# Kernel tuning notes

Hardware: AMD Instinct MI355X
Metric: run time of the kernel (lower is better)

## Reference

```python
import jax, jax.numpy as jnp
import numpy as np

NUM_HEADS = 8
KEY_DIM = 512  # d_gain = 1/sqrt(key_dim) in the original (NOT per-head dim)
MASK_FILL = -1000000.0


def setup_inputs() -> dict:
    key = jax.random.key(0)
    ks = jax.random.split(key, 6)
    N, Tq, Tk, D, U = 8, 1024, 1024, 512, 512
    query = jax.random.normal(ks[0], (N, Tq, D), dtype=jnp.float32)
    key_t = jax.random.normal(ks[1], (N, Tk, D), dtype=jnp.float32)
    key_mask = jax.random.randint(ks[2], (N, Tk), 0, 2).astype(bool)
    Wq = jax.random.normal(ks[3], (D, U), dtype=jnp.float32) / np.sqrt(D)
    Wk = jax.random.normal(ks[4], (D, U), dtype=jnp.float32) / np.sqrt(D)
    Wv = jax.random.normal(ks[5], (D, U), dtype=jnp.float32) / np.sqrt(D)
    return {"query": query, "key": key_t, "key_mask": key_mask,
            "Wq": Wq, "Wk": Wk, "Wv": Wv}


def reference(query, key, key_mask, Wq, Wk, Wv):
    N, Tq, _ = query.shape
    Tk = key.shape[1]
    U = Wq.shape[1]
    h = NUM_HEADS
    d = U // h
    scale = 1.0 / (KEY_DIM ** 0.5)

    # projections then split heads: [N,T,U] -> [h,N,T,d]
    q = (query @ Wq).reshape(N, Tq, h, d).transpose(2, 0, 1, 3)
    k = (key @ Wk).reshape(N, Tk, h, d).transpose(2, 0, 1, 3)
    v = (key @ Wv).reshape(N, Tk, h, d).transpose(2, 0, 1, 3)

    scores = scale * jnp.einsum('hnqd,hnkd->hnqk', q, k)
    scores = jnp.where(key_mask[None, :, None, :], scores, MASK_FILL)
    attn = jax.nn.softmax(scores, axis=3)
    out = jnp.einsum('hnqk,hnkd->hnqd', attn, v)
    # merge heads: [h,N,Tq,d] -> [N,Tq,h*d]
    return out.transpose(1, 2, 0, 3).reshape(N, Tq, U)
```

## Files before the change

### kernel.cpp

```cpp
#include <hip/hip_runtime.h>
#include <hip/hip_bf16.h>

typedef unsigned short u16;
typedef __attribute__((ext_vector_type(8))) short short8;
typedef __attribute__((ext_vector_type(4))) short short4v;
typedef __attribute__((ext_vector_type(4))) float f32x4;

#define NB 8
#define TT 1024
#define DD 512
#define UU 512
#define HH 8
#define DH 64
#define SCALE 0.044194173824159216f
#define LOG2E 1.4426950408889634f
#define MASK_FILL_2 -1442695.0f

__device__ __forceinline__ float ld_flex(const void* p, long i, bool f32) {
  if (f32) return ((const float*)p)[i];
  unsigned int u = (unsigned int)(((const u16*)p)[i]) << 16;
  return __uint_as_float(u);
}

__device__ __forceinline__ u16 f32_to_bf16(float f) {
  unsigned int u = __float_as_uint(f);
  unsigned int r = (u + 0x7FFFu + ((u >> 16) & 1u)) >> 16;
  return (u16)r;
}

__device__ __forceinline__ float ex2(float x) {
#if __has_builtin(__builtin_amdgcn_exp2f)
  return __builtin_amdgcn_exp2f(x);
#else
  return __expf(x * 0.6931471805599453f);
#endif
}

__device__ __forceinline__ unsigned int pk_bf16(float a, float b) {
  union { __hip_bfloat162 h2; unsigned int u; } c;
  c.h2 = __float22bfloat162_rn(make_float2(a, b));
  return c.u;
}

__device__ __forceinline__ void gld16(const void* g, void* l) {
  __builtin_amdgcn_global_load_lds(
      (const __attribute__((address_space(1))) unsigned int*)g,
      (__attribute__((address_space(3))) unsigned int*)l, 16, 0, 0);
}

#define CONV_BLOCKS 8192
#define WT_BLOCKS 768
#define MASK_BLOCKS 32

__global__ __launch_bounds__(256) void prep_kernel(
    const void* __restrict__ query, const void* __restrict__ key,
    const void* __restrict__ W0, const void* __restrict__ W1,
    const void* __restrict__ W2, const void* __restrict__ mask,
    u16* __restrict__ Xq, u16* __restrict__ Xk, u16* __restrict__ Wt,
    float* __restrict__ maskadd, int* __restrict__ flags) {
  __shared__ float tile[32][33];
  __shared__ int s_f32, s_mi32;
  const int b = blockIdx.x, tid = threadIdx.x;

  if (tid == 0) { s_f32 = 0; s_mi32 = 1; }
  __syncthreads();
  {
    const u16* qh = (const u16*)query;
    int weird = 0;
#pragma unroll
    for (int p = 0; p < 4; ++p) {
      unsigned int u = (unsigned int)qh[tid * 4 + p] << 16;
      float v = __uint_as_float(u);
      if (!(v == v) || fabsf(v) > 1e6f) weird = 1;
    }
    if (weird) atomicOr(&s_f32, 1);
    const unsigned int* mi = (const unsigned int*)mask;
    if (mi[tid * 2] > 1u || mi[tid * 2 + 1] > 1u) atomicAnd(&s_mi32, 0);
  }
  __syncthreads();
  const bool f32 = s_f32 != 0;
  const bool mi32 = s_mi32 != 0;
  if (b == CONV_BLOCKS && tid == 0) { flags[0] = s_f32; flags[1] = s_mi32; }

  if (b < CONV_BLOCKS) {
    if (!f32) return;
    const void* in = (b < 4096) ? query : key;
    u16* out = (b < 4096) ? Xq : Xk;
    int i = (b & 4095) * 256 + tid;
    float4 v = ((const float4*)in)[i];
    ushort4 o;
    o.x = f32_to_bf16(v.x); o.y = f32_to_bf16(v.y);
    o.z = f32_to_bf16(v.z); o.w = f32_to_bf16(v.w);
    ((ushort4*)out)[i] = o;
  } else if (b < CONV_BLOCKS + WT_BLOCKS) {
    const int lb = b - CONV_BLOCKS;
    const int z = lb >> 8, rem = lb & 255;
    const int k0 = (rem & 15) * 32, n0 = (rem >> 4) * 32;
    const void* W = (z == 0) ? W0 : (z == 1) ? W1 : W2;
    const float sc = (z == 0) ? SCALE * LOG2E : 1.0f;
    u16* out = Wt + (size_t)z * DD * UU;
#pragma unroll
    for (int p = 0; p < 4; ++p) {
      int i = (tid >> 5) + p * 8, j = tid & 31;
      tile[i][j] = ld_flex(W, (long)(k0 + i) * UU + n0 + j, f32);
    }
    __syncthreads();
#pragma unroll
    for (int p = 0; p < 4; ++p) {
      int nl = (tid >> 5) + p * 8, kl = tid & 31;
      out[(size_t)(n0 + nl) * DD + k0 + kl] = f32_to_bf16(tile[kl][nl] * sc);
    }
  } else {
    const int i = (b - CONV_BLOCKS - WT_BLOCKS) * 256 + tid;
    bool mv = mi32 ? (((const int*)mask)[i] != 0)
                   : (((const unsigned char*)mask)[i] != 0);
    maskadd[i] = mv ? 0.0f : MASK_FILL_2;
  }
}

__global__ __launch_bounds__(256) void proj_mfma(
    const void* __restrict__ query, const void* __restrict__ key,
    const u16* __restrict__ Xq, const u16* __restrict__ Xk,
    const u16* __restrict__ Wt, u16* __restrict__ Qp, u16* __restrict__ Kp,
    u16* __restrict__ Vt, const int* __restrict__ flags) {
  __shared__ __align__(16) u16 smem[128 * 136];
  u16* As = smem;
  u16* Bs = smem + 4096;
  const bool f32 = flags[0] != 0;
  const int z = blockIdx.z;
  const u16* X = (z == 0) ? (f32 ? Xq : (const u16*)query)
                          : (f32 ? Xk : (const u16*)key);
  const u16* Wz = Wt + (size_t)z * DD * UU;
  const int m0 = blockIdx.x * 128, n0 = blockIdx.y * 128;
  const int tid = threadIdx.x;
  const int w = tid >> 6, l = tid & 63;
  const int quad = l >> 4, l15 = l & 15;
  const int wm = (w >> 1) * 64, wn = (w & 1) * 64;

  const int c0 = w * 128 + l;
  const int row0 = c0 >> 2, q0 = (c0 & 3) * 8;
  const int c1 = c0 + 64;
  const int row1 = c1 >> 2, q1 = (c1 & 3) * 8;
  const u16* aS0 = X + (size_t)(m0 + row0) * DD + q0;
  const u16* aS1 = X + (size_t)(m0 + row1) * DD + q1;
  const u16* bS0 = Wz + (size_t)(n0 + row0) * DD + q0;
  const u16* bS1 = Wz + (size_t)(n0 + row1) * DD + q1;
  u16* aD0 = &As[(size_t)(w * 128) * 8];
  u16* aD1 = &As[(size_t)(w * 128 + 64) * 8];
  u16* bD0 = &Bs[(size_t)(w * 128) * 8];
  u16* bD1 = &Bs[(size_t)(w * 128 + 64) * 8];

  f32x4 acc[4][4];
#pragma unroll
  for (int mi = 0; mi < 4; ++mi)
#pragma unroll
    for (int ni = 0; ni < 4; ++ni)
#pragma unroll
      for (int r = 0; r < 4; ++r) acc[mi][ni][r] = 0.0f;

  for (int k0 = 0; k0 < DD; k0 += 32) {
    gld16(aS0 + k0, aD0);
    gld16(aS1 + k0, aD1);
    gld16(bS0 + k0, bD0);
    gld16(bS1 + k0, bD1);
    __syncthreads();
    short8 af[4], bf[4];
#pragma unroll
    for (int mi = 0; mi < 4; ++mi)
      af[mi] = *(const short8*)&As[(wm + mi * 16 + l15) * 32 + quad * 8];
#pragma unroll
    for (int ni = 0; ni < 4; ++ni)
      bf[ni] = *(const short8*)&Bs[(wn + ni * 16 + l15) * 32 + quad * 8];
#pragma unroll
    for (int mi = 0; mi < 4; ++mi)
#pragma unroll
      for (int ni = 0; ni < 4; ++ni)
        acc[mi][ni] = __builtin_amdgcn_mfma_f32_16x16x32_bf16(
            af[mi], bf[ni], acc[mi][ni], 0, 0, 0);
    __syncthreads();
  }

  if (z < 2) {
#pragma unroll
    for (int mi = 0; mi < 4; ++mi)
#pragma unroll
      for (int ni = 0; ni < 4; ++ni) {
        const int ml = wm + mi * 16 + quad * 4;
        const int nl = wn + ni * 16 + l15;
#pragma unroll
        for (int r = 0; r < 4; ++r)
          smem[(ml + r) * 136 + nl] = f32_to_bf16(acc[mi][ni][r]);
      }
  } else {
#pragma unroll
    for (int mi = 0; mi < 4; ++mi)
#pragma unroll
      for (int ni = 0; ni < 4; ++ni) {
        const int ml = wm + mi * 16 + quad * 4;
        const int nl = wn + ni * 16 + l15;
        ushort4 pk;
        pk.x = f32_to_bf16(acc[mi][ni][0]);
        pk.y = f32_to_bf16(acc[mi][ni][1]);
        pk.z = f32_to_bf16(acc[mi][ni][2]);
        pk.w = f32_to_bf16(acc[mi][ni][3]);
        *(ushort4*)&smem[nl * 136 + ml] = pk;
      }
  }
  __syncthreads();

  if (z < 2) {
    u16* outp = (z == 0) ? Qp : Kp;
#pragma unroll
    for (int p = 0; p < 8; ++p) {
      const int idx = tid + p * 256;
      const int row = idx >> 4, c8 = (idx & 15) * 8;
      short8 v = *(const short8*)&smem[row * 136 + c8];
      *(short8*)&outp[(size_t)(m0 + row) * UU + n0 + c8] = v;
    }
  } else {
    const int nb = m0 >> 10, tk0 = m0 & 1023;
#pragma unroll
    for (int p = 0; p < 8; ++p) {
      const int idx = tid + p * 256;
      const int row = idx >> 4, c8 = (idx & 15) * 8;
      const int u = n0 + row, h = u >> 6, dh = u & 63;
      short8 v = *(const short8*)&smem[row * 136 + c8];
      *(short8*)&Vt[(size_t)((nb * HH + h) * DH + dh) * TT + tk0 + c8] = v;
    }
  }
}

__global__ __launch_bounds__(256) void attn_mfma(
    const u16* __restrict__ Qp, const u16* __restrict__ Kp,
    const u16* __restrict__ Vt, const float* __restrict__ maskadd,
    void* __restrict__ out, const int* __restrict__ flags) {
  __shared__ __align__(16) char smem[23040];
  const int tid = threadIdx.x;
  const int w = tid >> 6, l = tid & 63;
  const int quad = l >> 4, l15 = l & 15;
  const int lid = blockIdx.x + (blockIdx.y << 4) + (blockIdx.z << 7);
  const int swz = (lid & 7) * 128 + (lid >> 3);
  const int qt = swz & 15, h = (swz >> 4) & 7, n = swz >> 7;
  const int qsub = w >> 1, ks = w & 1;
  const int q0 = qt * 64 + qsub * 32;
  const int kb0 = ks * 512;
  const bool f32o = flags[0] != 0;
  u16* Pw = (u16*)smem + w * 2304;
  float* lp = (float*)(smem + 18432);
  float* s_mask = (float*)(smem + 18944);

  ((float4*)s_mask)[tid] = ((const float4*)(maskadd + n * TT))[tid];

  const u16* qbase = Qp + (size_t)(n * TT + q0 + l15) * UU + h * DH + quad * 8;
  short8 bq[2][2];
  bq[0][0] = *(const short8*)(qbase);
  bq[0][1] = *(const short8*)(qbase + 32);
  bq[1][0] = *(const short8*)(qbase + 16 * UU);
  bq[1][1] = *(const short8*)(qbase + 16 * UU + 32);

  const u16* kbase = Kp + (size_t)(n * TT + l15) * UU + h * DH + quad * 8;
  const u16* vbase = Vt + (size_t)((n * HH + h) * DH + l15) * TT + quad * 8;

  f32x4 o[2][4];
  float lsum[2] = {0.0f, 0.0f};
#pragma unroll
  for (int nq = 0; nq < 2; ++nq)
#pragma unroll
    for (int ni = 0; ni < 4; ++ni)
#pragma unroll
      for (int r = 0; r < 4; ++r) o[nq][ni][r] = 0.0f;

  __syncthreads();

  short8 ak[2][2];
#pragma unroll
  for (int kt = 0; kt < 2; ++kt)
#pragma unroll
    for (int kd = 0; kd < 2; ++kd)
      ak[kt][kd] = *(const short8*)(kbase + (size_t)(kb0 + kt * 16) * UU + kd * 32);
  {
    f32x4 s[2][2];
#pragma unroll
    for (int kt = 0; kt < 2; ++kt)
#pragma unroll
      for (int nq = 0; nq < 2; ++nq) {
#pragma unroll
        for (int r = 0; r < 4; ++r) s[kt][nq][r] = 0.0f;
#pragma unroll
        for (int kd = 0; kd < 2; ++kd)
          s[kt][nq] = __builtin_amdgcn_mfma_f32_16x16x32_bf16(
              ak[kt][kd], bq[nq][kd], s[kt][nq], 0, 0, 0);
      }
#pragma unroll
    for (int kt = 0; kt < 2; ++kt)
#pragma unroll
      for (int kd = 0; kd < 2; ++kd)
        ak[kt][kd] = *(const short8*)(kbase + (size_t)(kb0 + 32 + kt * 16) * UU + kd * 32);
    float4 mk[2];
    mk[0] = *(const float4*)&s_mask[kb0 + quad * 4];
    mk[1] = *(const float4*)&s_mask[kb0 + 16 + quad * 4];
#pragma unroll
    for (int kt = 0; kt < 2; ++kt)
#pragma unroll
      for (int nq = 0; nq < 2; ++nq) {
        float e0 = ex2(s[kt][nq][0] + mk[kt].x);
        float e1 = ex2(s[kt][nq][1] + mk[kt].y);
        float e2 = ex2(s[kt][nq][2] + mk[kt].z);
        float e3 = ex2(s[kt][nq][3] + mk[kt].w);
        lsum[nq] += (e0 + e1) + (e2 + e3);
        uint2 pk = make_uint2(pk_bf16(e0, e1), pk_bf16(e2, e3));
        *(uint2*)&Pw[(nq * 16 + l15) * 36 + kt * 16 + quad * 4] = pk;
      }
  }

#pragma unroll 1
  for (int it = 0; it < 16; ++it) {
    const int kb = kb0 + it * 32;
    u16* Pr = Pw + (it & 1) * 1152;
    short8 ap[2];
#pragma unroll
    for (int nq = 0; nq < 2; ++nq) {
      short4v lo = *(const short4v*)&Pr[(nq * 16 + l15) * 36 + quad * 8];
      short4v hi = *(const short4v*)&Pr[(nq * 16 + l15) * 36 + quad * 8 + 4];
      union { short8 v8; short4v v4[2]; } u;
      u.v4[0] = lo; u.v4[1] = hi;
      ap[nq] = u.v8;
    }
    short8 vf[4];
#pragma unroll
    for (int ni = 0; ni < 4; ++ni)
      vf[ni] = *(const short8*)(vbase + (size_t)(ni * 16) * TT + kb);
    __builtin_amdgcn_sched_barrier(0);

    if (it < 15) {
      f32x4 s[2][2];
#pragma unroll
      for (int kt = 0; kt < 2; ++kt)
#pragma unroll
        for (int nq = 0; nq < 2; ++nq) {
#pragma unroll
          for (int r = 0; r < 4; ++r) s[kt][nq][r] = 0.0f;
#pragma unroll
          for (int kd = 0; kd < 2; ++kd)
            s[kt][nq] = __builtin_amdgcn_mfma_f32_16x16x32_bf16(
                ak[kt][kd], bq[nq][kd], s[kt][nq], 0, 0, 0);
        }
      if (it < 14) {
        const int kb2 = kb + 64;
#pragma unroll
        for (int kt = 0; kt < 2; ++kt)
#pragma unroll
          for (int kd = 0; kd < 2; ++kd)
            ak[kt][kd] = *(const short8*)(kbase + (size_t)(kb2 + kt * 16) * UU + kd * 32);
      }
      float4 mk[2];
      mk[0] = *(const float4*)&s_mask[kb + 32 + quad * 4];
      mk[1] = *(const float4*)&s_mask[kb + 48 + quad * 4];
      u16* Pn = Pw + ((it + 1) & 1) * 1152;
#pragma unroll
      for (int kt = 0; kt < 2; ++kt)
#pragma unroll
        for (int nq = 0; nq < 2; ++nq) {
          float e0 = ex2(s[kt][nq][0] + mk[kt].x);
          float e1 = ex2(s[kt][nq][1] + mk[kt].y);
          float e2 = ex2(s[kt][nq][2] + mk[kt].z);
          float e3 = ex2(s[kt][nq][3] + mk[kt].w);
          lsum[nq] += (e0 + e1) + (e2 + e3);
          uint2 pk = make_uint2(pk_bf16(e0, e1), pk_bf16(e2, e3));
          *(uint2*)&Pn[(nq * 16 + l15) * 36 + kt * 16 + quad * 4] = pk;
        }
    }
    __builtin_amdgcn_sched_barrier(0);

#pragma unroll
    for (int nq = 0; nq < 2; ++nq)
#pragma unroll
      for (int ni = 0; ni < 4; ++ni)
        o[nq][ni] = __builtin_amdgcn_mfma_f32_16x16x32_bf16(
            ap[nq], vf[ni], o[nq][ni], 0, 0, 0);
  }

#pragma unroll
  for (int nq = 0; nq < 2; ++nq) {
    lsum[nq] += __shfl_xor(lsum[nq], 16);
    lsum[nq] += __shfl_xor(lsum[nq], 32);
  }

  if (quad == 0) {
    lp[w * 32 + l15] = lsum[0];
    lp[w * 32 + 16 + l15] = lsum[1];
  }
  __syncthreads();

  float* cbuf = (float*)smem;
#pragma unroll
  for (int c = 0; c < 4; ++c) {
    if ((w >> 1) == (c >> 1)) {
      float* Ow = cbuf + (w & 1) * (16 * 68);
#pragma unroll
      for (int ni = 0; ni < 4; ++ni)
#pragma unroll
        for (int r = 0; r < 4; ++r)
          Ow[(quad * 4 + r) * 68 + ni * 16 + l15] = o[c & 1][ni][r];
    }
    __syncthreads();
    for (int i = tid; i < 16 * 64; i += 256) {
      int q = i >> 6, j = i & 63;
      float s = cbuf[q * 68 + j] + cbuf[1088 + q * 68 + j];
      int qg = c * 16 + q;
      int base = (c >> 1) * 64;
      float lsum2 = lp[base + (qg & 31)] + lp[base + 32 + (qg & 31)];
      float v = s / lsum2;
      size_t idx = (size_t)(n * TT + qt * 64 + qg) * UU + h * DH + j;
      if (f32o) ((float*)out)[idx] = v;
      else ((u16*)out)[idx] = f32_to_bf16(v);
    }
    __syncthreads();
  }
}

extern "C" void kernel_launch(void* const* d_in, const int* in_sizes, int n_in,
                              void* d_out, int out_size, void* d_ws, size_t ws_size,
                              hipStream_t stream) {
  const void* query = d_in[0];
  const void* key   = d_in[1];
  const void* mask  = d_in[2];
  const void* Wq    = d_in[3];
  const void* Wk    = d_in[4];
  const void* Wv    = d_in[5];

  char* base = (char*)d_ws;
  int* flags = (int*)base;
  float* maskadd = (float*)(base + 256);
  u16* Wt  = (u16*)(base + 64 * 1024);
  u16* Xq  = Wt + (size_t)3 * DD * UU;
  u16* Xk  = Xq + (size_t)NB * TT * DD;
  u16* Qp  = Xk + (size_t)NB * TT * DD;
  u16* Kp  = Qp + (size_t)NB * TT * UU;
  u16* Vtp = Kp + (size_t)NB * TT * UU;

  prep_kernel<<<CONV_BLOCKS + WT_BLOCKS + MASK_BLOCKS, 256, 0, stream>>>(
      query, key, Wq, Wk, Wv, mask, Xq, Xk, Wt, maskadd, flags);

  dim3 pgrid(NB * TT / 128, UU / 128, 3);
  proj_mfma<<<pgrid, 256, 0, stream>>>(query, key, Xq, Xk, Wt, Qp, Kp, Vtp, flags);

  dim3 agrid(TT / 64, HH, NB);
  attn_mfma<<<agrid, 256, 0, stream>>>(Qp, Kp, Vtp, maskadd, d_out, flags);
}
```

Measured before the change: 183.6 us.

## Double-buffer LDS loads in projection GEMM and swizzle block order

The projection GEMM now double-buffers its A/B tiles in shared memory. The next k-slice's global-to-LDS loads are issued before computing the current slice, with explicit vmcnt waits and raw barriers, so memory latency can overlap with MFMA work. Block indices are also remapped through a swizzle meant to improve L2 locality across blocks that share weight and input tiles. This uses the full 34KB smem buffer, relies on manual waitcnt correctness, and the swizzle hard-codes the grid shape (64x4x3).

```diff
diff --git a/kernel.cpp b/kernel.cpp
--- a/kernel.cpp
+++ b/kernel.cpp
@@ -124,14 +124,14 @@
     const u16* __restrict__ Wt, u16* __restrict__ Qp, u16* __restrict__ Kp,
     u16* __restrict__ Vt, const int* __restrict__ flags) {
   __shared__ __align__(16) u16 smem[128 * 136];
-  u16* As = smem;
-  u16* Bs = smem + 4096;
   const bool f32 = flags[0] != 0;
-  const int z = blockIdx.z;
+  const int lid = blockIdx.x + (blockIdx.y << 6) + (blockIdx.z << 8);
+  const int swz = (lid & 7) * 96 + (lid >> 3);
+  const int bx = swz & 63, by = (swz >> 6) & 3, z = swz >> 8;
   const u16* X = (z == 0) ? (f32 ? Xq : (const u16*)query)
                           : (f32 ? Xk : (const u16*)key);
   const u16* Wz = Wt + (size_t)z * DD * UU;
-  const int m0 = blockIdx.x * 128, n0 = blockIdx.y * 128;
+  const int m0 = bx * 128, n0 = by * 128;
   const int tid = threadIdx.x;
   const int w = tid >> 6, l = tid & 63;
   const int quad = l >> 4, l15 = l & 15;
@@ -145,10 +145,8 @@
   const u16* aS1 = X + (size_t)(m0 + row1) * DD + q1;
   const u16* bS0 = Wz + (size_t)(n0 + row0) * DD + q0;
   const u16* bS1 = Wz + (size_t)(n0 + row1) * DD + q1;
-  u16* aD0 = &As[(size_t)(w * 128) * 8];
-  u16* aD1 = &As[(size_t)(w * 128 + 64) * 8];
-  u16* bD0 = &Bs[(size_t)(w * 128) * 8];
-  u16* bD1 = &Bs[(size_t)(w * 128 + 64) * 8];
+  const int dD0 = w * 1024;
+  const int dD1 = w * 1024 + 512;
 
   f32x4 acc[4][4];
 #pragma unroll
@@ -158,26 +156,41 @@
 #pragma unroll
       for (int r = 0; r < 4; ++r) acc[mi][ni][r] = 0.0f;
 
-  for (int k0 = 0; k0 < DD; k0 += 32) {
-    gld16(aS0 + k0, aD0);
-    gld16(aS1 + k0, aD1);
-    gld16(bS0 + k0, bD0);
-    gld16(bS1 + k0, bD1);
-    __syncthreads();
+  gld16(aS0, smem + dD0);
+  gld16(aS1, smem + dD1);
+  gld16(bS0, smem + 4096 + dD0);
+  gld16(bS1, smem + 4096 + dD1);
+
+#pragma unroll 1
+  for (int t = 0; t < 16; ++t) {
+    const int co = (t & 1) * 8192;
+    if (t < 15) {
+      const int k1 = (t + 1) * 32;
+      const int no = ((t + 1) & 1) * 8192;
+      gld16(aS0 + k1, smem + no + dD0);
+      gld16(aS1 + k1, smem + no + dD1);
+      gld16(bS0 + k1, smem + no + 4096 + dD0);
+      gld16(bS1 + k1, smem + no + 4096 + dD1);
+      asm volatile("s_waitcnt vmcnt(4)" ::: "memory");
+    } else {
+      asm volatile("s_waitcnt vmcnt(0)" ::: "memory");
+    }
+    __builtin_amdgcn_s_barrier();
+
     short8 af[4], bf[4];
 #pragma unroll
     for (int mi = 0; mi < 4; ++mi)
-      af[mi] = *(const short8*)&As[(wm + mi * 16 + l15) * 32 + quad * 8];
+      af[mi] = *(const short8*)&smem[co + (wm + mi * 16 + l15) * 32 + quad * 8];
 #pragma unroll
     for (int ni = 0; ni < 4; ++ni)
-      bf[ni] = *(const short8*)&Bs[(wn + ni * 16 + l15) * 32 + quad * 8];
+      bf[ni] = *(const short8*)&smem[co + 4096 + (wn + ni * 16 + l15) * 32 + quad * 8];
 #pragma unroll
     for (int mi = 0; mi < 4; ++mi)
 #pragma unroll
       for (int ni = 0; ni < 4; ++ni)
         acc[mi][ni] = __builtin_amdgcn_mfma_f32_16x16x32_bf16(
             af[mi], bf[ni], acc[mi][ni], 0, 0, 0);
-    __syncthreads();
+    __builtin_amdgcn_s_barrier();
   }
 
   if (z < 2) {
```

Result: no change. 180.5 us (-1.7%).
